# Kernel optimization log

Hardware: AMD Instinct MI355X
Metric: run time of the kernel (lower is better)

## Reference

```python
import jax, jax.numpy as jnp
import numpy as np

QMAX = 7.0   # int4 symmetric, narrow range [-7, 7] per weight; acts use [-8, 7]
QMIN = -8.0

def _ste_quant(v, scale, qmin, qmax):
    """Symmetric per-tensor fake-quant with straight-through estimator."""
    s = jax.lax.stop_gradient(scale)
    q = jnp.clip(jnp.round(v / s), qmin, qmax) * s
    return v + jax.lax.stop_gradient(q - v)


def setup_inputs() -> dict:
    key = jax.random.key(0)
    k1, k2, k3 = jax.random.split(key, 3)
    d_model, vocab = 1024, 50257
    x = jax.random.normal(k1, (2, 1024, d_model), jnp.float32)
    W = jax.random.normal(k2, (vocab, d_model), jnp.float32) * 0.02
    b = jax.random.normal(k3, (vocab,), jnp.float32) * 0.01
    return {"x": x, "W": W, "b": b}


def reference(x, W, b):
    # Activation quant: 4-bit signed, per-tensor scale from max-abs stats
    sx = jnp.max(jnp.abs(x)) / QMAX
    xq = _ste_quant(x, sx, QMIN, QMAX)
    # Weight quant: 4-bit signed per-tensor
    sw = jnp.max(jnp.abs(W)) / QMAX
    wq = _ste_quant(W, sw, QMIN, QMAX)
    # Int32 bias: quantized at the accumulator scale sx*sw (range huge -> round only)
    sb = jax.lax.stop_gradient(sx * sw)
    bq = b + jax.lax.stop_gradient(jnp.round(b / sb) * sb - b)
    # Quantized GEMM with int32-style accumulation, expressed as dequantized matmul
    logits = jnp.einsum('bsd,vd->bsv', xq, wq) + bq  # [B, S, vocab]
    return jax.nn.log_softmax(logits, axis=-1)
```

## Files before the change

kernel.cpp:

```cpp
#include <hip/hip_runtime.h>
#include <hip/hip_bf16.h>

#define N_VOCAB 50257
#define NB      393
#define N_PAD   50304
#define D_K     1024
#define M_ROWS  2048
#define GEMM_BLOCKS (NB * 16)
#define PER_XCD     (GEMM_BLOCKS/8)

typedef __attribute__((ext_vector_type(4))) int i32x4;

__device__ inline void async_copy16(const void* g, void* l) {
  auto* gp = (const __attribute__((address_space(1))) unsigned int*)g;
  auto* lp = (__attribute__((address_space(3))) unsigned int*)l;
  __builtin_amdgcn_global_load_lds(gp, lp, 16, 0, 0);
}

__device__ inline unsigned long long q8(float v, float s) {
  float q = fminf(fmaxf(rintf(v / s), -8.f), 7.f);
  return (unsigned long long)(unsigned char)(signed char)(int)q;
}

__global__ __launch_bounds__(256) void absmax2_kernel(
    const float4* __restrict__ x, int nx4, const float4* __restrict__ Wp,
    int nw4, unsigned* __restrict__ amax) {
  const bool isx = blockIdx.x < 512;
  const float4* p = isx ? x : Wp;
  const int n4 = isx ? nx4 : nw4;
  const int b0 = isx ? blockIdx.x : blockIdx.x - 512;
  const int nb = isx ? 512 : (gridDim.x - 512);
  float m = 0.f;
  for (int i = b0 * blockDim.x + threadIdx.x; i < n4; i += nb * blockDim.x) {
    float4 v = p[i];
    m = fmaxf(m, fmaxf(fmaxf(fabsf(v.x), fabsf(v.y)),
                       fmaxf(fabsf(v.z), fabsf(v.w))));
  }
#pragma unroll
  for (int off = 32; off; off >>= 1) m = fmaxf(m, __shfl_xor(m, off));
  __shared__ float red[4];
  int tid = threadIdx.x;
  if ((tid & 63) == 0) red[tid >> 6] = m;
  __syncthreads();
  if (tid == 0) {
    m = fmaxf(fmaxf(red[0], red[1]), fmaxf(red[2], red[3]));
    atomicMax(&amax[isx ? 0 : 1], __float_as_uint(m));
  }
}

#define XB8  1024
#define WB8  25152
__global__ __launch_bounds__(256) void quant_kernel(
    const float4* __restrict__ x, const float4* __restrict__ Wp,
    const float* __restrict__ b, unsigned long long* __restrict__ qx,
    unsigned long long* __restrict__ qw, float* __restrict__ bq,
    const unsigned* __restrict__ amax) {
  const int bid = blockIdx.x;
  const int tid = threadIdx.x;
  if (bid < XB8) {
    int i = bid * 256 + tid;
    float s = __uint_as_float(amax[0]) * (1.0f / 7.0f);
    float4 a = x[2 * i], c = x[2 * i + 1];
    qx[i] = q8(a.x, s) | q8(a.y, s) << 8 | q8(a.z, s) << 16 |
            q8(a.w, s) << 24 | q8(c.x, s) << 32 | q8(c.y, s) << 40 |
            q8(c.z, s) << 48 | q8(c.w, s) << 56;
  } else if (bid < XB8 + WB8) {
    int i = (bid - XB8) * 256 + tid;
    unsigned long long v = 0ull;
    if (i < N_VOCAB * (D_K / 8)) {
      float s = __uint_as_float(amax[1]) * (1.0f / 7.0f);
      float4 a = Wp[2 * i], c = Wp[2 * i + 1];
      v = q8(a.x, s) | q8(a.y, s) << 8 | q8(a.z, s) << 16 | q8(a.w, s) << 24 |
          q8(c.x, s) << 32 | q8(c.y, s) << 40 | q8(c.z, s) << 48 |
          q8(c.w, s) << 56;
    }
    qw[i] = v;
  } else {
    int i = (bid - (XB8 + WB8)) * 256 + tid;
    if (i < N_PAD) {
      float v = 0.f;
      if (i < N_VOCAB) {
        float sb = (__uint_as_float(amax[0]) * (1.0f / 7.0f)) *
                   (__uint_as_float(amax[1]) * (1.0f / 7.0f));
        v = rintf(b[i] / sb) * sb;
      }
      bq[i] = v;
    }
  }
}

__global__ __launch_bounds__(256, 4) void gemm_kernel(
    const signed char* __restrict__ qx,
    const signed char* __restrict__ qw,
    const float* __restrict__ bq,
    const unsigned* __restrict__ amax,
    float* __restrict__ outp,
    float* __restrict__ pmax,
    float* __restrict__ psum)
{
  constexpr int BK = 64;
  constexpr int NT = D_K / BK;
  __shared__ __align__(16) signed char sA[2][128 * BK];
  __shared__ __align__(16) signed char sB[3][128 * BK];

  const int tid = threadIdx.x;
  const int l = tid & 63;
  const int w = tid >> 6;
  const int wr = w >> 1, wc = w & 1;

  const int bid = blockIdx.x;
  const int vb = (bid & 7) * PER_XCD + (bid >> 3);
  const int nb = vb >> 4;
  const int m0 = (vb & 15) * 128;
  const int n0 = nb * 128;

  const float sx = __uint_as_float(amax[0]) * (1.0f / 7.0f);
  const float sw = __uint_as_float(amax[1]) * (1.0f / 7.0f);
  const float scale = sx * sw;

  i32x4 acc[4][4] = {};

  const int srow = l >> 2;
  const int scol = ((l & 3) ^ ((l >> 3) & 3)) * 16;

  auto stageA = [&](int buf, int kt) {
    int k0 = kt * BK;
#pragma unroll
    for (int i = 0; i < 2; ++i) {
      int c = w * 2 + i;
      int row = c * 16 + srow;
      async_copy16(qx + (size_t)(m0 + row) * D_K + k0 + scol,
                   &sA[buf][c * 1024]);
    }
  };
  auto stageB = [&](int buf, int kt) {
    int k0 = kt * BK;
#pragma unroll
    for (int i = 0; i < 2; ++i) {
      int c = w * 2 + i;
      int row = c * 16 + srow;
      async_copy16(qw + (size_t)(n0 + row) * D_K + k0 + scol,
                   &sB[buf][c * 1024]);
    }
  };

  stageA(0, 0);
  stageB(0, 0);
  stageB(1, 1);
  asm volatile("s_waitcnt vmcnt(2)" ::: "memory");
  __builtin_amdgcn_s_barrier();
  __builtin_amdgcn_sched_barrier(0);

#pragma unroll
  for (int kt = 0; kt < NT; ++kt) {
    const int ca = kt & 1;
    const int cb = kt % 3;

    i32x4 af[4], bfr[4];
#pragma unroll
    for (int mi = 0; mi < 4; ++mi) {
      int row = wr * 64 + mi * 16 + (l & 15);
      int kb = ((l >> 4) ^ ((row >> 1) & 3)) * 16;
      af[mi] = *(const i32x4*)&sA[ca][row * BK + kb];
    }
#pragma unroll
    for (int ni = 0; ni < 4; ++ni) {
      int row = wc * 64 + ni * 16 + (l & 15);
      int kb = ((l >> 4) ^ ((row >> 1) & 3)) * 16;
      bfr[ni] = *(const i32x4*)&sB[cb][row * BK + kb];
    }

    if (kt + 1 < NT) stageA(ca ^ 1, kt + 1);
    if (kt + 2 < NT) stageB((kt + 2) % 3, kt + 2);

    __builtin_amdgcn_s_setprio(1);
#pragma unroll
    for (int mi = 0; mi < 4; ++mi)
#pragma unroll
      for (int ni = 0; ni < 4; ++ni)
        acc[mi][ni] = __builtin_amdgcn_mfma_i32_16x16x64_i8(
            af[mi], bfr[ni], acc[mi][ni], 0, 0, 0);
    __builtin_amdgcn_s_setprio(0);
    __builtin_amdgcn_sched_barrier(0);

    if (kt + 1 < NT) {
      if (kt + 2 < NT)
        asm volatile("s_waitcnt vmcnt(2)" ::: "memory");
      else
        asm volatile("s_waitcnt vmcnt(0)" ::: "memory");
      __builtin_amdgcn_s_barrier();
      __builtin_amdgcn_sched_barrier(0);
    }
  }

  bool valid[4];
  float bb[4];
#pragma unroll
  for (int ni = 0; ni < 4; ++ni) {
    int col = n0 + wc * 64 + ni * 16 + (l & 15);
    valid[ni] = (col < N_VOCAB);
    bb[ni] = valid[ni] ? bq[col] : 0.f;
  }
  float lg[4][4][4];
#pragma unroll
  for (int mi = 0; mi < 4; ++mi)
#pragma unroll
    for (int ni = 0; ni < 4; ++ni)
#pragma unroll
      for (int r = 0; r < 4; ++r)
        lg[mi][ni][r] = (float)acc[mi][ni][r] * scale + bb[ni];

  __syncthreads();
  float* redMax = (float*)&sB[0][0];
  float* redSum = redMax + 256;

  float rmax[4][4];
#pragma unroll
  for (int mi = 0; mi < 4; ++mi)
#pragma unroll
    for (int r = 0; r < 4; ++r) {
      float mval = -3.4e38f;
#pragma unroll
      for (int ni = 0; ni < 4; ++ni)
        if (valid[ni]) mval = fmaxf(mval, lg[mi][ni][r]);
#pragma unroll
      for (int off = 1; off < 16; off <<= 1)
        mval = fmaxf(mval, __shfl_xor(mval, off));
      rmax[mi][r] = mval;
      if ((l & 15) == 0)
        redMax[(wr * 64 + mi * 16 + (l >> 4) * 4 + r) * 2 + wc] = mval;
    }
  __syncthreads();

#pragma unroll
  for (int mi = 0; mi < 4; ++mi)
#pragma unroll
    for (int r = 0; r < 4; ++r) {
      int rl = wr * 64 + mi * 16 + (l >> 4) * 4 + r;
      float gmax = fmaxf(redMax[rl * 2 + 0], redMax[rl * 2 + 1]);
      float s = 0.f;
#pragma unroll
      for (int ni = 0; ni < 4; ++ni)
        if (valid[ni]) s += __expf(lg[mi][ni][r] - gmax);
#pragma unroll
      for (int off = 1; off < 16; off <<= 1)
        s += __shfl_xor(s, off);
      if ((l & 15) == 0) redSum[rl * 2 + wc] = s;
      rmax[mi][r] = gmax;
    }
  __syncthreads();

  if (wc == 0 && (l & 15) == 0) {
#pragma unroll
    for (int mi = 0; mi < 4; ++mi)
#pragma unroll
      for (int r = 0; r < 4; ++r) {
        int rl = wr * 64 + mi * 16 + (l >> 4) * 4 + r;
        int rowg = m0 + rl;
        pmax[(size_t)rowg * NB + nb] = rmax[mi][r];
        psum[(size_t)rowg * NB + nb] = redSum[rl * 2 + 0] + redSum[rl * 2 + 1];
      }
  }

#pragma unroll
  for (int mi = 0; mi < 4; ++mi)
#pragma unroll
    for (int r = 0; r < 4; ++r) {
      int rowg = m0 + wr * 64 + mi * 16 + (l >> 4) * 4 + r;
      size_t rb = (size_t)rowg * N_VOCAB;
#pragma unroll
      for (int ni = 0; ni < 4; ++ni) {
        if (valid[ni]) {
          int col = n0 + wc * 64 + ni * 16 + (l & 15);
          outp[rb + col] = lg[mi][ni][r];
        }
      }
    }
}

__global__ __launch_bounds__(256) void logz_sub_kernel(
    const float* __restrict__ pmax, const float* __restrict__ psum,
    float* __restrict__ out) {
  const int row = blockIdx.x >> 2;
  const int part = blockIdx.x & 3;
  const float* pm = pmax + (size_t)row * NB;
  const float* ps = psum + (size_t)row * NB;
  const int tid = threadIdx.x;
  __shared__ float red[9];

  float m = -3.4e38f;
  for (int i = tid; i < NB; i += 256) m = fmaxf(m, pm[i]);
#pragma unroll
  for (int off = 32; off; off >>= 1) m = fmaxf(m, __shfl_xor(m, off));
  if ((tid & 63) == 0) red[tid >> 6] = m;
  __syncthreads();
  m = fmaxf(fmaxf(red[0], red[1]), fmaxf(red[2], red[3]));

  float s = 0.f;
  for (int i = tid; i < NB; i += 256) s += ps[i] * __expf(pm[i] - m);
#pragma unroll
  for (int off = 32; off; off >>= 1) s += __shfl_xor(s, off);
  if ((tid & 63) == 0) red[4 + (tid >> 6)] = s;
  __syncthreads();
  if (tid == 0) {
    s = red[4] + red[5] + red[6] + red[7];
    red[8] = m + __logf(s);
  }
  __syncthreads();
  const float lz = red[8];

  const size_t base = (size_t)row * N_VOCAB;
  const int a = (4 - (row & 3)) & 3;
  const int n4 = (N_VOCAB - a) >> 2;
  const int p4 = (n4 + 3) >> 2;
  const int i0 = part * p4;
  const int i1 = min(n4, i0 + p4);
  float4* p = (float4*)(out + base + a);
  for (int i = i0 + tid; i < i1; i += 256) {
    float4 v = p[i];
    v.x -= lz; v.y -= lz; v.z -= lz; v.w -= lz;
    p[i] = v;
  }
  if (part == 0) {
    if (tid < a) out[base + tid] -= lz;
  } else if (part == 3) {
    const int done = a + n4 * 4;
    if (tid < N_VOCAB - done) out[base + done + tid] -= lz;
  }
}

extern "C" void kernel_launch(void* const* d_in, const int* in_sizes, int n_in,
                              void* d_out, int out_size, void* d_ws,
                              size_t ws_size, hipStream_t stream) {
  const float* x = (const float*)d_in[0];
  const float* W = (const float*)d_in[1];
  const float* b = (const float*)d_in[2];
  float* out = (float*)d_out;

  char* ws = (char*)d_ws;
  unsigned* amax = (unsigned*)ws;
  float* bq = (float*)(ws + 4096);
  float* pmax = (float*)(ws + (2ull << 20));
  float* psum = (float*)(ws + (6ull << 20));
  signed char* qx = (signed char*)(ws + (10ull << 20));
  signed char* qw = (signed char*)(ws + (14ull << 20));

  hipMemsetAsync(amax, 0, 8, stream);

  const int nx4 = (M_ROWS * D_K) / 4;
  const int nw4 = (N_VOCAB * D_K) / 4;

  absmax2_kernel<<<512 + 4096, 256, 0, stream>>>((const float4*)x, nx4,
                                                 (const float4*)W, nw4, amax);

  quant_kernel<<<XB8 + WB8 + 197, 256, 0, stream>>>(
      (const float4*)x, (const float4*)W, b, (unsigned long long*)qx,
      (unsigned long long*)qw, bq, amax);

  gemm_kernel<<<GEMM_BLOCKS, 256, 0, stream>>>(qx, qw, bq, amax, out, pmax,
                                               psum);

  logz_sub_kernel<<<M_ROWS * 4, 256, 0, stream>>>(pmax, psum, out);
}
```

Before: 533.9 us.

## Use 512-thread GEMM blocks with 2x4 wave grid and smaller per-wave tiles

The GEMM block grows from 4 to 8 waves, arranged as a 2x4 wave grid over the same 128x128 output tile. Each wave now computes 64x32 with 8 accumulators instead of 16, and each thread issues one async copy per operand per stage. The softmax partial reductions are widened to combine four column-waves. The aim is more waves to hide latency and less register pressure, at the cost of lower MFMA work per LDS fragment load and more synchronisation overhead per block.

```diff
diff --git a/kernel.cpp b/kernel.cpp
--- a/kernel.cpp
+++ b/kernel.cpp
@@ -89,7 +89,7 @@
   }
 }
 
-__global__ __launch_bounds__(256, 4) void gemm_kernel(
+__global__ __launch_bounds__(512, 6) void gemm_kernel(
     const signed char* __restrict__ qx,
     const signed char* __restrict__ qw,
     const float* __restrict__ bq,
@@ -106,7 +106,8 @@
   const int tid = threadIdx.x;
   const int l = tid & 63;
   const int w = tid >> 6;
-  const int wr = w >> 1, wc = w & 1;
+  const int wr = w >> 2;
+  const int wc = w & 3;
 
   const int bid = blockIdx.x;
   const int vb = (bid & 7) * PER_XCD + (bid >> 3);
@@ -118,36 +119,26 @@
   const float sw = __uint_as_float(amax[1]) * (1.0f / 7.0f);
   const float scale = sx * sw;
 
-  i32x4 acc[4][4] = {};
+  i32x4 acc[4][2] = {};
 
   const int srow = l >> 2;
   const int scol = ((l & 3) ^ ((l >> 3) & 3)) * 16;
 
   auto stageA = [&](int buf, int kt) {
-    int k0 = kt * BK;
-#pragma unroll
-    for (int i = 0; i < 2; ++i) {
-      int c = w * 2 + i;
-      int row = c * 16 + srow;
-      async_copy16(qx + (size_t)(m0 + row) * D_K + k0 + scol,
-                   &sA[buf][c * 1024]);
-    }
+    int row = w * 16 + srow;
+    async_copy16(qx + (size_t)(m0 + row) * D_K + kt * BK + scol,
+                 &sA[buf][w * 1024]);
   };
   auto stageB = [&](int buf, int kt) {
-    int k0 = kt * BK;
-#pragma unroll
-    for (int i = 0; i < 2; ++i) {
-      int c = w * 2 + i;
-      int row = c * 16 + srow;
-      async_copy16(qw + (size_t)(n0 + row) * D_K + k0 + scol,
-                   &sB[buf][c * 1024]);
-    }
+    int row = w * 16 + srow;
+    async_copy16(qw + (size_t)(n0 + row) * D_K + kt * BK + scol,
+                 &sB[buf][w * 1024]);
   };
 
   stageA(0, 0);
   stageB(0, 0);
   stageB(1, 1);
-  asm volatile("s_waitcnt vmcnt(2)" ::: "memory");
+  asm volatile("s_waitcnt vmcnt(1)" ::: "memory");
   __builtin_amdgcn_s_barrier();
   __builtin_amdgcn_sched_barrier(0);
 
@@ -156,7 +147,7 @@
     const int ca = kt & 1;
     const int cb = kt % 3;
 
-    i32x4 af[4], bfr[4];
+    i32x4 af[4], bfr[2];
 #pragma unroll
     for (int mi = 0; mi < 4; ++mi) {
       int row = wr * 64 + mi * 16 + (l & 15);
@@ -164,8 +155,8 @@
       af[mi] = *(const i32x4*)&sA[ca][row * BK + kb];
     }
 #pragma unroll
-    for (int ni = 0; ni < 4; ++ni) {
-      int row = wc * 64 + ni * 16 + (l & 15);
+    for (int ni = 0; ni < 2; ++ni) {
+      int row = wc * 32 + ni * 16 + (l & 15);
       int kb = ((l >> 4) ^ ((row >> 1) & 3)) * 16;
       bfr[ni] = *(const i32x4*)&sB[cb][row * BK + kb];
     }
@@ -177,7 +168,7 @@
 #pragma unroll
     for (int mi = 0; mi < 4; ++mi)
 #pragma unroll
-      for (int ni = 0; ni < 4; ++ni)
+      for (int ni = 0; ni < 2; ++ni)
         acc[mi][ni] = __builtin_amdgcn_mfma_i32_16x16x64_i8(
             af[mi], bfr[ni], acc[mi][ni], 0, 0, 0);
     __builtin_amdgcn_s_setprio(0);
@@ -185,7 +176,7 @@
 
     if (kt + 1 < NT) {
       if (kt + 2 < NT)
-        asm volatile("s_waitcnt vmcnt(2)" ::: "memory");
+        asm volatile("s_waitcnt vmcnt(1)" ::: "memory");
       else
         asm volatile("s_waitcnt vmcnt(0)" ::: "memory");
       __builtin_amdgcn_s_barrier();
@@ -193,26 +184,26 @@
     }
   }
 
-  bool valid[4];
-  float bb[4];
-#pragma unroll
-  for (int ni = 0; ni < 4; ++ni) {
-    int col = n0 + wc * 64 + ni * 16 + (l & 15);
+  bool valid[2];
+  float bb[2];
+#pragma unroll
+  for (int ni = 0; ni < 2; ++ni) {
+    int col = n0 + wc * 32 + ni * 16 + (l & 15);
     valid[ni] = (col < N_VOCAB);
     bb[ni] = valid[ni] ? bq[col] : 0.f;
   }
-  float lg[4][4][4];
+  float lg[4][2][4];
 #pragma unroll
   for (int mi = 0; mi < 4; ++mi)
 #pragma unroll
-    for (int ni = 0; ni < 4; ++ni)
+    for (int ni = 0; ni < 2; ++ni)
 #pragma unroll
       for (int r = 0; r < 4; ++r)
         lg[mi][ni][r] = (float)acc[mi][ni][r] * scale + bb[ni];
 
   __syncthreads();
   float* redMax = (float*)&sB[0][0];
-  float* redSum = redMax + 256;
+  float* redSum = redMax + 512;
 
   float rmax[4][4];
 #pragma unroll
@@ -221,14 +212,14 @@
     for (int r = 0; r < 4; ++r) {
       float mval = -3.4e38f;
 #pragma unroll
-      for (int ni = 0; ni < 4; ++ni)
+      for (int ni = 0; ni < 2; ++ni)
         if (valid[ni]) mval = fmaxf(mval, lg[mi][ni][r]);
 #pragma unroll
       for (int off = 1; off < 16; off <<= 1)
         mval = fmaxf(mval, __shfl_xor(mval, off));
       rmax[mi][r] = mval;
       if ((l & 15) == 0)
-        redMax[(wr * 64 + mi * 16 + (l >> 4) * 4 + r) * 2 + wc] = mval;
+        redMax[(wr * 64 + mi * 16 + (l >> 4) * 4 + r) * 4 + wc] = mval;
     }
   __syncthreads();
 
@@ -237,15 +228,16 @@
 #pragma unroll
     for (int r = 0; r < 4; ++r) {
       int rl = wr * 64 + mi * 16 + (l >> 4) * 4 + r;
-      float gmax = fmaxf(redMax[rl * 2 + 0], redMax[rl * 2 + 1]);
+      float gmax = fmaxf(fmaxf(redMax[rl * 4 + 0], redMax[rl * 4 + 1]),
+                         fmaxf(redMax[rl * 4 + 2], redMax[rl * 4 + 3]));
       float s = 0.f;
 #pragma unroll
-      for (int ni = 0; ni < 4; ++ni)
+      for (int ni = 0; ni < 2; ++ni)
         if (valid[ni]) s += __expf(lg[mi][ni][r] - gmax);
 #pragma unroll
       for (int off = 1; off < 16; off <<= 1)
         s += __shfl_xor(s, off);
-      if ((l & 15) == 0) redSum[rl * 2 + wc] = s;
+      if ((l & 15) == 0) redSum[rl * 4 + wc] = s;
       rmax[mi][r] = gmax;
     }
   __syncthreads();
@@ -258,7 +250,9 @@
         int rl = wr * 64 + mi * 16 + (l >> 4) * 4 + r;
         int rowg = m0 + rl;
         pmax[(size_t)rowg * NB + nb] = rmax[mi][r];
-        psum[(size_t)rowg * NB + nb] = redSum[rl * 2 + 0] + redSum[rl * 2 + 1];
+        psum[(size_t)rowg * NB + nb] =
+            (redSum[rl * 4 + 0] + redSum[rl * 4 + 1]) +
+            (redSum[rl * 4 + 2] + redSum[rl * 4 + 3]);
       }
   }
 
@@ -269,9 +263,9 @@
       int rowg = m0 + wr * 64 + mi * 16 + (l >> 4) * 4 + r;
       size_t rb = (size_t)rowg * N_VOCAB;
 #pragma unroll
-      for (int ni = 0; ni < 4; ++ni) {
+      for (int ni = 0; ni < 2; ++ni) {
         if (valid[ni]) {
-          int col = n0 + wc * 64 + ni * 16 + (l & 15);
+          int col = n0 + wc * 32 + ni * 16 + (l & 15);
           outp[rb + col] = lg[mi][ni][r];
         }
       }
@@ -357,7 +351,7 @@
       (const float4*)x, (const float4*)W, b, (unsigned long long*)qx,
       (unsigned long long*)qw, bq, amax);
 
-  gemm_kernel<<<GEMM_BLOCKS, 256, 0, stream>>>(qx, qw, bq, amax, out, pmax,
+  gemm_kernel<<<GEMM_BLOCKS, 512, 0, stream>>>(qx, qw, bq, amax, out, pmax,
                                                psum);
 
   logz_sub_kernel<<<M_ROWS * 4, 256, 0, stream>>>(pmax, psum, out);
```

New measurement: 574.8 us. 7.7% more time.
